# Kernel optimization log

Hardware: AMD Instinct MI355X
Metric: run time of the kernel (lower is better)

Reference implementation:

```python
import jax, jax.numpy as jnp
import numpy as np

D_MODEL = 1024
N_HEADS = 16
D_HEAD = D_MODEL // N_HEADS
WINDOW = 256
SCALE = D_HEAD ** -0.5


def setup_inputs() -> dict:
    key = jax.random.key(0)
    ks = jax.random.split(key, 5)
    B, S = 2, 2048
    x = jax.random.normal(ks[0], (B, S, D_MODEL), dtype=jnp.float32)
    # weights stored as [d_in, d_out] so forward is x @ W + b
    W_qkv = jax.random.normal(ks[1], (D_MODEL, 3 * D_MODEL), dtype=jnp.float32) * (D_MODEL ** -0.5)
    b_qkv = jnp.zeros((3 * D_MODEL,), dtype=jnp.float32)
    W_out = jax.random.normal(ks[2], (D_MODEL, D_MODEL), dtype=jnp.float32) * (D_MODEL ** -0.5)
    b_out = jnp.zeros((D_MODEL,), dtype=jnp.float32)
    return {"x": x, "W_qkv": W_qkv, "b_qkv": b_qkv, "W_out": W_out, "b_out": b_out}


def _window_mask(S):
    # Faithful to source: keep positions where (i <= j) & (i >= j - WINDOW + 1),
    # i = query index (rows), j = key index (cols). (Anti-causal window, as in repo.)
    idx = jnp.arange(S)
    keep = (idx[:, None] <= idx[None, :]) & (idx[:, None] >= idx[None, :] - WINDOW + 1)
    return keep  # [S, S] bool


def reference(x, W_qkv, b_qkv, W_out, b_out):
    B, S, D = x.shape
    qkv = x @ W_qkv + b_qkv                      # [B,S,3D]
    q, k, v = jnp.split(qkv, 3, axis=-1)
    def heads(t):
        return t.reshape(B, S, N_HEADS, D_HEAD).transpose(0, 2, 1, 3)  # [B,H,S,dh]
    q, k, v = heads(q), heads(k), heads(v)
    attn = jnp.einsum('bhid,bhjd->bhij', q, k) * SCALE  # [B,H,S,S]
    keep = _window_mask(S)
    attn = jnp.where(keep[None, None], attn, -jnp.inf)
    attn = jax.nn.softmax(attn, axis=-1)
    # dropout is identity in eval mode
    out = jnp.einsum('bhij,bhjd->bhid', attn, v)        # [B,H,S,dh]
    out = out.transpose(0, 2, 1, 3).reshape(B, S, D)
    return out @ W_out + b_out
```

## Files before the change

### kernel.cpp

```cpp
#include <hip/hip_runtime.h>

typedef __bf16 bf16x8 __attribute__((ext_vector_type(8)));
typedef float f32x4 __attribute__((ext_vector_type(4)));
typedef unsigned short u16x8 __attribute__((ext_vector_type(8)));
typedef unsigned short u16x4 __attribute__((ext_vector_type(4)));

#define MFMA16(a, b, c) __builtin_amdgcn_mfma_f32_16x16x32_bf16((a), (b), (c), 0, 0, 0)

#define WAIT_VM2  asm volatile("s_waitcnt vmcnt(2)" ::: "memory")
#define WAIT_VM0  asm volatile("s_waitcnt vmcnt(0)" ::: "memory")
#define WAIT_LGKM asm volatile("s_waitcnt lgkmcnt(0)" ::: "memory")
#define BAR       __builtin_amdgcn_s_barrier()

__device__ __forceinline__ unsigned short f2bf(float f) {
  union { float f; unsigned int i; } v; v.f = f;
  unsigned int u = v.i;
  u += 0x7fffu + ((u >> 16) & 1u);
  return (unsigned short)(u >> 16);
}

__device__ __forceinline__ void gload16(const void* g, void* l) {
  __builtin_amdgcn_global_load_lds(
      (const __attribute__((address_space(1))) unsigned int*)g,
      (__attribute__((address_space(3))) unsigned int*)l, 16, 0, 0);
}

__global__ __launch_bounds__(256) void convert_x(const float* __restrict__ X,
                                                 unsigned short* __restrict__ Xb) {
  size_t i = (size_t)(blockIdx.x * 256 + threadIdx.x) * 8;
  f32x4 f0 = *(const f32x4*)(X + i);
  f32x4 f1 = *(const f32x4*)(X + i + 4);
  u16x8 t;
#pragma unroll
  for (int j = 0; j < 4; ++j) { t[j] = f2bf(f0[j]); t[4 + j] = f2bf(f1[j]); }
  *(u16x8*)(Xb + i) = t;
}

__global__ __launch_bounds__(256) void transpose_w(const float* __restrict__ W,
                                                   unsigned short* __restrict__ Wt,
                                                   int N) {
  __shared__ unsigned short t[32][33];
  int tx = threadIdx.x & 31, ty = threadIdx.x >> 5;
  int bx = blockIdx.x;
  int by = blockIdx.y;
#pragma unroll
  for (int j = 0; j < 4; ++j) {
    int r = ty + j * 8;
    t[tx][r] = f2bf(W[(size_t)(by * 32 + r) * N + bx * 32 + tx]);
  }
  __syncthreads();
#pragma unroll
  for (int j = 0; j < 4; ++j) {
    int r = ty + j * 8;
    Wt[(size_t)(bx * 32 + r) * 1024 + by * 32 + tx] = t[r][tx];
  }
}

__global__ __launch_bounds__(512) void gemm_bt(
    const unsigned short* __restrict__ A, const unsigned short* __restrict__ Bt,
    const float* __restrict__ bias,
    unsigned short* __restrict__ O0, unsigned short* __restrict__ O1,
    unsigned short* __restrict__ O2, float* __restrict__ OF, int mode) {
  __shared__ __align__(16) unsigned short As0[128 * 32];
  __shared__ __align__(16) unsigned short Bs0[128 * 32];
  __shared__ __align__(16) unsigned short As1[128 * 32];
  __shared__ __align__(16) unsigned short Bs1[128 * 32];

  const int K = 1024;
  int tid = threadIdx.x;
  int lane = tid & 63, wave = tid >> 6, quad = lane >> 4, l16 = lane & 15;
  int wr = wave >> 2, wc = wave & 3;
  int m0 = blockIdx.x * 128, n0 = blockIdx.y * 128;

  int srow = tid >> 2, su = tid & 3;
  const unsigned short* ag = A + (size_t)(m0 + srow) * K + su * 8;
  const unsigned short* bg = Bt + (size_t)(n0 + srow) * K + su * 8;
  int loff = tid * 16;

  int abase = (wr * 64 + l16) * 64 + quad * 16;
  int bbase = (wc * 32 + l16) * 64 + quad * 16;

  f32x4 acc[4][2];
#pragma unroll
  for (int i = 0; i < 4; ++i)
#pragma unroll
    for (int j = 0; j < 2; ++j) acc[i][j] = f32x4{0.f, 0.f, 0.f, 0.f};

  auto STAGE = [&](int k0, char* Asb, char* Bsb) {
    gload16(ag + k0, Asb + loff);
    gload16(bg + k0, Bsb + loff);
  };
  auto COMPUTE = [&](const char* Asb, const char* Bsb) {
    bf16x8 af[4], bfr[2];
#pragma unroll
    for (int t = 0; t < 4; ++t)
      af[t] = *(const bf16x8*)(Asb + abase + t * 1024);
#pragma unroll
    for (int t = 0; t < 2; ++t)
      bfr[t] = *(const bf16x8*)(Bsb + bbase + t * 1024);
#pragma unroll
    for (int mt = 0; mt < 4; ++mt)
#pragma unroll
      for (int nt = 0; nt < 2; ++nt)
        acc[mt][nt] = MFMA16(af[mt], bfr[nt], acc[mt][nt]);
  };

  STAGE(0, (char*)As0, (char*)Bs0);
  for (int t = 0; t < 30; t += 2) {
    STAGE((t + 1) * 32, (char*)As1, (char*)Bs1);
    WAIT_VM2; BAR;
    COMPUTE((const char*)As0, (const char*)Bs0);
    WAIT_LGKM; BAR;
    STAGE((t + 2) * 32, (char*)As0, (char*)Bs0);
    WAIT_VM2; BAR;
    COMPUTE((const char*)As1, (const char*)Bs1);
    WAIT_LGKM; BAR;
  }
  STAGE(31 * 32, (char*)As1, (char*)Bs1);
  WAIT_VM2; BAR;
  COMPUTE((const char*)As0, (const char*)Bs0);
  WAIT_LGKM; BAR;
  WAIT_VM0; BAR;
  COMPUTE((const char*)As1, (const char*)Bs1);

  if (mode == 0) {
#pragma unroll
    for (int nt = 0; nt < 2; ++nt) {
      int n = n0 + wc * 32 + nt * 16 + l16;
      float bv = bias[n];
      int seg = n >> 10, cc = n & 1023, hh = cc >> 6, d = cc & 63;
#pragma unroll
      for (int mt = 0; mt < 4; ++mt) {
        int mb = m0 + wr * 64 + mt * 16 + quad * 4;
        int b = mb >> 11, s = mb & 2047;
        if (seg == 2) {
          u16x4 pk;
#pragma unroll
          for (int r = 0; r < 4; ++r) pk[r] = f2bf(acc[mt][nt][r] + bv);
          *(u16x4*)&O2[((size_t)((b << 4) + hh) * 64 + d) * 2048 + s] = pk;
        } else {
          unsigned short* O = seg ? O1 : O0;
#pragma unroll
          for (int r = 0; r < 4; ++r)
            O[((size_t)((b << 4) + hh) * 2048 + (s + r)) * 64 + d] = f2bf(acc[mt][nt][r] + bv);
        }
      }
    }
  } else {
#pragma unroll
    for (int nt = 0; nt < 2; ++nt) {
      int n = n0 + wc * 32 + nt * 16 + l16;
      float bv = bias[n];
#pragma unroll
      for (int mt = 0; mt < 4; ++mt) {
        int mb = m0 + wr * 64 + mt * 16 + quad * 4;
#pragma unroll
        for (int r = 0; r < 4; ++r)
          OF[(size_t)(mb + r) * 1024 + n] = acc[mt][nt][r] + bv;
      }
    }
  }
}

__global__ __launch_bounds__(256) void gemm_bt64(
    const unsigned short* __restrict__ A, const unsigned short* __restrict__ Bt,
    const float* __restrict__ bias, float* __restrict__ OF) {
  __shared__ __align__(16) unsigned short As0[64 * 32];
  __shared__ __align__(16) unsigned short Bs0[64 * 32];
  __shared__ __align__(16) unsigned short As1[64 * 32];
  __shared__ __align__(16) unsigned short Bs1[64 * 32];

  const int K = 1024;
  int tid = threadIdx.x;
  int lane = tid & 63, wave = tid >> 6, quad = lane >> 4, l16 = lane & 15;
  int wr = wave >> 1, wc = wave & 1;
  int m0 = blockIdx.x * 64, n0 = blockIdx.y * 64;

  int srow = tid >> 2, su = tid & 3;
  const unsigned short* ag = A + (size_t)(m0 + srow) * K + su * 8;
  const unsigned short* bg = Bt + (size_t)(n0 + srow) * K + su * 8;
  int loff = tid * 16;

  int abase = (wr * 32 + l16) * 64 + quad * 16;
  int bbase = (wc * 32 + l16) * 64 + quad * 16;

  f32x4 acc[2][2];
#pragma unroll
  for (int i = 0; i < 2; ++i)
#pragma unroll
    for (int j = 0; j < 2; ++j) acc[i][j] = f32x4{0.f, 0.f, 0.f, 0.f};

  auto STAGE = [&](int k0, char* Asb, char* Bsb) {
    gload16(ag + k0, Asb + loff);
    gload16(bg + k0, Bsb + loff);
  };
  auto COMPUTE = [&](const char* Asb, const char* Bsb) {
    bf16x8 af[2], bfr[2];
#pragma unroll
    for (int t = 0; t < 2; ++t) {
      af[t]  = *(const bf16x8*)(Asb + abase + t * 1024);
      bfr[t] = *(const bf16x8*)(Bsb + bbase + t * 1024);
    }
#pragma unroll
    for (int mt = 0; mt < 2; ++mt)
#pragma unroll
      for (int nt = 0; nt < 2; ++nt)
        acc[mt][nt] = MFMA16(af[mt], bfr[nt], acc[mt][nt]);
  };

  STAGE(0, (char*)As0, (char*)Bs0);
  for (int t = 0; t < 30; t += 2) {
    STAGE((t + 1) * 32, (char*)As1, (char*)Bs1);
    WAIT_VM2; BAR;
    COMPUTE((const char*)As0, (const char*)Bs0);
    WAIT_LGKM; BAR;
    STAGE((t + 2) * 32, (char*)As0, (char*)Bs0);
    WAIT_VM2; BAR;
    COMPUTE((const char*)As1, (const char*)Bs1);
    WAIT_LGKM; BAR;
  }
  STAGE(31 * 32, (char*)As1, (char*)Bs1);
  WAIT_VM2; BAR;
  COMPUTE((const char*)As0, (const char*)Bs0);
  WAIT_LGKM; BAR;
  WAIT_VM0; BAR;
  COMPUTE((const char*)As1, (const char*)Bs1);

#pragma unroll
  for (int nt = 0; nt < 2; ++nt) {
    int n = n0 + wc * 32 + nt * 16 + l16;
    float bv = bias[n];
#pragma unroll
    for (int mt = 0; mt < 2; ++mt) {
      int mb = m0 + wr * 32 + mt * 16 + quad * 4;
#pragma unroll
      for (int r = 0; r < 4; ++r)
        OF[(size_t)(mb + r) * 1024 + n] = acc[mt][nt][r] + bv;
    }
  }
}

__global__ __launch_bounds__(256) void attn_kernel(
    const unsigned short* __restrict__ Q, const unsigned short* __restrict__ Kq,
    const unsigned short* __restrict__ Vt, unsigned short* __restrict__ AO) {
  __shared__ __align__(16) unsigned short Ps[4][16][40];

  int bid = blockIdx.x;
  int qblk = bid & 31, h = (bid >> 5) & 15, b = bid >> 9;
  int q0 = qblk * 64;
  int tid = threadIdx.x, lane = tid & 63, wave = tid >> 6, quad = lane >> 4, l16 = lane & 15;

  const unsigned short* Qb = Q + (size_t)(((b << 4) + h) * 2048) * 64;
  const unsigned short* Kb = Kq + (size_t)(((b << 4) + h) * 2048) * 64;
  const unsigned short* Vb = Vt + (size_t)(((b << 4) + h) * 64) * 2048;

  int qrow = q0 + wave * 16 + l16;
  bf16x8 qf0 = __builtin_bit_cast(bf16x8, *(const u16x8*)&Qb[(size_t)qrow * 64 + quad * 8]);
  bf16x8 qf1 = __builtin_bit_cast(bf16x8, *(const u16x8*)&Qb[(size_t)qrow * 64 + 32 + quad * 8]);

  float mrow[4], lrow[4];
  f32x4 zero = {0.f, 0.f, 0.f, 0.f};
  f32x4 o[4];
#pragma unroll
  for (int i = 0; i < 4; ++i) o[i] = zero;
#pragma unroll
  for (int r = 0; r < 4; ++r) { mrow[r] = -1e30f; lrow[r] = 0.f; }

  const float SCALE = 0.125f;
  int pstart = (wave >= 2) ? 1 : 0;
  int pend = pstart + 8;

  for (int p = pstart; p <= pend; ++p) {
    int kbase = q0 + p * 32;

    f32x4 sc[2];
    __builtin_amdgcn_s_setprio(1);
#pragma unroll
    for (int t = 0; t < 2; ++t) {
      int krow = kbase + t * 16 + l16;
      krow = krow > 2047 ? 2047 : krow;
      bf16x8 kf0 = __builtin_bit_cast(bf16x8, *(const u16x8*)&Kb[(size_t)krow * 64 + quad * 8]);
      bf16x8 kf1 = __builtin_bit_cast(bf16x8, *(const u16x8*)&Kb[(size_t)krow * 64 + 32 + quad * 8]);
      f32x4 z = zero;
      z = MFMA16(qf0, kf0, z);
      z = MFMA16(qf1, kf1, z);
      sc[t] = z;
    }
    __builtin_amdgcn_s_setprio(0);

    float sv[2][4];
#pragma unroll
    for (int t = 0; t < 2; ++t)
#pragma unroll
      for (int r = 0; r < 4; ++r) {
        int kg = kbase + t * 16 + l16;
        int qg = q0 + wave * 16 + quad * 4 + r;
        bool valid = (kg >= qg) && (kg <= qg + 255) && (kg < 2048);
        sv[t][r] = valid ? sc[t][r] * SCALE : -1e30f;
      }
#pragma unroll
    for (int r = 0; r < 4; ++r) {
      float v = fmaxf(sv[0][r], sv[1][r]);
      v = fmaxf(v, __shfl_xor(v, 1));
      v = fmaxf(v, __shfl_xor(v, 2));
      v = fmaxf(v, __shfl_xor(v, 4));
      v = fmaxf(v, __shfl_xor(v, 8));
      float mnew = fmaxf(mrow[r], v);
      float alpha = __expf(mrow[r] - mnew);
      mrow[r] = mnew;
      float p0 = __expf(sv[0][r] - mnew);
      float p1 = __expf(sv[1][r] - mnew);
      p0 = (sv[0][r] > -5e29f) ? p0 : 0.f;
      p1 = (sv[1][r] > -5e29f) ? p1 : 0.f;
      float rs = p0 + p1;
      rs += __shfl_xor(rs, 1);
      rs += __shfl_xor(rs, 2);
      rs += __shfl_xor(rs, 4);
      rs += __shfl_xor(rs, 8);
      lrow[r] = lrow[r] * alpha + rs;
#pragma unroll
      for (int nt = 0; nt < 4; ++nt) o[nt][r] *= alpha;
      Ps[wave][quad * 4 + r][l16] = f2bf(p0);
      Ps[wave][quad * 4 + r][16 + l16] = f2bf(p1);
    }
    __threadfence_block();
    bf16x8 pf = __builtin_bit_cast(bf16x8, *(const u16x8*)&Ps[wave][l16][quad * 8]);

    int vcol = kbase + quad * 8;
    vcol = vcol > 2040 ? 2040 : vcol;
    __builtin_amdgcn_s_setprio(1);
#pragma unroll
    for (int nt = 0; nt < 4; ++nt) {
      int vrow = nt * 16 + l16;
      bf16x8 vf = __builtin_bit_cast(bf16x8, *(const u16x8*)&Vb[(size_t)vrow * 2048 + vcol]);
      o[nt] = MFMA16(pf, vf, o[nt]);
    }
    __builtin_amdgcn_s_setprio(0);
  }

  unsigned short* dst = AO + ((size_t)(b * 2048 + q0 + wave * 16) * 1024) + h * 64;
#pragma unroll
  for (int nt = 0; nt < 4; ++nt)
#pragma unroll
    for (int r = 0; r < 4; ++r) {
      int qq = quad * 4 + r;
      dst[(size_t)qq * 1024 + nt * 16 + l16] = f2bf(o[nt][r] / lrow[r]);
    }
}

extern "C" void kernel_launch(void* const* d_in, const int* in_sizes, int n_in,
                              void* d_out, int out_size, void* d_ws, size_t ws_size,
                              hipStream_t stream) {
  const float* x = (const float*)d_in[0];
  const float* W_qkv = (const float*)d_in[1];
  const float* b_qkv = (const float*)d_in[2];
  const float* W_out = (const float*)d_in[3];
  const float* b_out = (const float*)d_in[4];
  float* out = (float*)d_out;

  unsigned short* ws = (unsigned short*)d_ws;
  unsigned short* Qw  = ws;
  unsigned short* Kw  = ws + 4194304;
  unsigned short* Vw  = ws + 8388608;
  unsigned short* Wqt = ws + 12582912;
  unsigned short* AO  = ws + 12582912;
  unsigned short* Wot = ws;
  unsigned short* Xb  = (unsigned short*)d_out;

  dim3 blk(256);
  dim3 gblk(512);
  convert_x<<<dim3(2048), blk, 0, stream>>>(x, Xb);
  transpose_w<<<dim3(96, 32), blk, 0, stream>>>(W_qkv, Wqt, 3072);
  gemm_bt<<<dim3(32, 24), gblk, 0, stream>>>(Xb, Wqt, b_qkv, Qw, Kw, Vw, nullptr, 0);
  attn_kernel<<<dim3(1024), blk, 0, stream>>>(Qw, Kw, Vw, AO);
  transpose_w<<<dim3(32, 32), blk, 0, stream>>>(W_out, Wot, 1024);
  gemm_bt64<<<dim3(64, 16), blk, 0, stream>>>(AO, Wot, b_out, out);
}
```

Measured before the change: 175.7 us.

## Transpose score MFMA so each lane owns one query row; prefetch V earlier

The QK^T MFMA operands are swapped so the score tile comes out transposed, with each lane holding one query row's scores across keys. The online softmax max and sum then need only two cross-lane shuffles instead of four per row, and per-row alpha is broadcast with shuffles. V fragments are loaded before the softmax to hide their global-load latency. The transposed probabilities are written to LDS as packed 4-element vectors, and the final row sums are exchanged through LDS for normalization. This costs extra shuffles for alpha and an LDS round trip at the end.

```diff
diff --git a/kernel.cpp b/kernel.cpp
--- a/kernel.cpp
+++ b/kernel.cpp
@@ -254,17 +254,15 @@
   const unsigned short* Kb = Kq + (size_t)(((b << 4) + h) * 2048) * 64;
   const unsigned short* Vb = Vt + (size_t)(((b << 4) + h) * 64) * 2048;
 
-  int qrow = q0 + wave * 16 + l16;
-  bf16x8 qf0 = __builtin_bit_cast(bf16x8, *(const u16x8*)&Qb[(size_t)qrow * 64 + quad * 8]);
-  bf16x8 qf1 = __builtin_bit_cast(bf16x8, *(const u16x8*)&Qb[(size_t)qrow * 64 + 32 + quad * 8]);
-
-  float mrow[4], lrow[4];
+  int qg = q0 + wave * 16 + l16;
+  bf16x8 qf0 = __builtin_bit_cast(bf16x8, *(const u16x8*)&Qb[(size_t)qg * 64 + quad * 8]);
+  bf16x8 qf1 = __builtin_bit_cast(bf16x8, *(const u16x8*)&Qb[(size_t)qg * 64 + 32 + quad * 8]);
+
+  float m = -1e30f, l = 0.f;
   f32x4 zero = {0.f, 0.f, 0.f, 0.f};
   f32x4 o[4];
 #pragma unroll
   for (int i = 0; i < 4; ++i) o[i] = zero;
-#pragma unroll
-  for (int r = 0; r < 4; ++r) { mrow[r] = -1e30f; lrow[r] = 0.f; }
 
   const float SCALE = 0.125f;
   int pstart = (wave >= 2) ? 1 : 0;
@@ -282,61 +280,83 @@
       bf16x8 kf0 = __builtin_bit_cast(bf16x8, *(const u16x8*)&Kb[(size_t)krow * 64 + quad * 8]);
       bf16x8 kf1 = __builtin_bit_cast(bf16x8, *(const u16x8*)&Kb[(size_t)krow * 64 + 32 + quad * 8]);
       f32x4 z = zero;
-      z = MFMA16(qf0, kf0, z);
-      z = MFMA16(qf1, kf1, z);
+      z = MFMA16(kf0, qf0, z);
+      z = MFMA16(kf1, qf1, z);
       sc[t] = z;
     }
     __builtin_amdgcn_s_setprio(0);
 
+    bf16x8 vf[4];
+    {
+      int vcol = kbase + quad * 8;
+      vcol = vcol > 2040 ? 2040 : vcol;
+#pragma unroll
+      for (int nt = 0; nt < 4; ++nt)
+        vf[nt] = __builtin_bit_cast(bf16x8,
+            *(const u16x8*)&Vb[(size_t)(nt * 16 + l16) * 2048 + vcol]);
+    }
+
     float sv[2][4];
 #pragma unroll
     for (int t = 0; t < 2; ++t)
 #pragma unroll
       for (int r = 0; r < 4; ++r) {
-        int kg = kbase + t * 16 + l16;
-        int qg = q0 + wave * 16 + quad * 4 + r;
+        int kg = kbase + t * 16 + quad * 4 + r;
         bool valid = (kg >= qg) && (kg <= qg + 255) && (kg < 2048);
         sv[t][r] = valid ? sc[t][r] * SCALE : -1e30f;
       }
-#pragma unroll
-    for (int r = 0; r < 4; ++r) {
-      float v = fmaxf(sv[0][r], sv[1][r]);
-      v = fmaxf(v, __shfl_xor(v, 1));
-      v = fmaxf(v, __shfl_xor(v, 2));
-      v = fmaxf(v, __shfl_xor(v, 4));
-      v = fmaxf(v, __shfl_xor(v, 8));
-      float mnew = fmaxf(mrow[r], v);
-      float alpha = __expf(mrow[r] - mnew);
-      mrow[r] = mnew;
-      float p0 = __expf(sv[0][r] - mnew);
-      float p1 = __expf(sv[1][r] - mnew);
-      p0 = (sv[0][r] > -5e29f) ? p0 : 0.f;
-      p1 = (sv[1][r] > -5e29f) ? p1 : 0.f;
-      float rs = p0 + p1;
-      rs += __shfl_xor(rs, 1);
-      rs += __shfl_xor(rs, 2);
-      rs += __shfl_xor(rs, 4);
-      rs += __shfl_xor(rs, 8);
-      lrow[r] = lrow[r] * alpha + rs;
-#pragma unroll
-      for (int nt = 0; nt < 4; ++nt) o[nt][r] *= alpha;
-      Ps[wave][quad * 4 + r][l16] = f2bf(p0);
-      Ps[wave][quad * 4 + r][16 + l16] = f2bf(p1);
+
+    float vmax = fmaxf(fmaxf(fmaxf(sv[0][0], sv[0][1]), fmaxf(sv[0][2], sv[0][3])),
+                       fmaxf(fmaxf(sv[1][0], sv[1][1]), fmaxf(sv[1][2], sv[1][3])));
+    vmax = fmaxf(vmax, __shfl_xor(vmax, 16));
+    vmax = fmaxf(vmax, __shfl_xor(vmax, 32));
+    float mnew = fmaxf(m, vmax);
+    float alpha = __expf(m - mnew);
+    m = mnew;
+    float pe[2][4];
+#pragma unroll
+    for (int t = 0; t < 2; ++t)
+#pragma unroll
+      for (int r = 0; r < 4; ++r) {
+        float e = __expf(sv[t][r] - mnew);
+        pe[t][r] = (sv[t][r] > -5e29f) ? e : 0.f;
+      }
+    float rs = ((pe[0][0] + pe[0][1]) + (pe[0][2] + pe[0][3])) +
+               ((pe[1][0] + pe[1][1]) + (pe[1][2] + pe[1][3]));
+    rs += __shfl_xor(rs, 16);
+    rs += __shfl_xor(rs, 32);
+    l = l * alpha + rs;
+
+    f32x4 av;
+#pragma unroll
+    for (int r = 0; r < 4; ++r) av[r] = __shfl(alpha, quad * 4 + r);
+#pragma unroll
+    for (int nt = 0; nt < 4; ++nt) o[nt] *= av;
+
+#pragma unroll
+    for (int t = 0; t < 2; ++t) {
+      u16x4 pk;
+#pragma unroll
+      for (int r = 0; r < 4; ++r) pk[r] = f2bf(pe[t][r]);
+      *(u16x4*)&Ps[wave][l16][t * 16 + quad * 4] = pk;
     }
     __threadfence_block();
     bf16x8 pf = __builtin_bit_cast(bf16x8, *(const u16x8*)&Ps[wave][l16][quad * 8]);
 
-    int vcol = kbase + quad * 8;
-    vcol = vcol > 2040 ? 2040 : vcol;
     __builtin_amdgcn_s_setprio(1);
 #pragma unroll
-    for (int nt = 0; nt < 4; ++nt) {
-      int vrow = nt * 16 + l16;
-      bf16x8 vf = __builtin_bit_cast(bf16x8, *(const u16x8*)&Vb[(size_t)vrow * 2048 + vcol]);
-      o[nt] = MFMA16(pf, vf, o[nt]);
-    }
+    for (int nt = 0; nt < 4; ++nt)
+      o[nt] = MFMA16(pf, vf[nt], o[nt]);
     __builtin_amdgcn_s_setprio(0);
   }
+
+  __threadfence_block();
+  float* Lf = (float*)&Ps[wave][0][0];
+  Lf[l16] = l;
+  __threadfence_block();
+  float lr[4];
+#pragma unroll
+  for (int r = 0; r < 4; ++r) lr[r] = Lf[quad * 4 + r];
 
   unsigned short* dst = AO + ((size_t)(b * 2048 + q0 + wave * 16) * 1024) + h * 64;
 #pragma unroll
@@ -344,7 +364,7 @@
 #pragma unroll
     for (int r = 0; r < 4; ++r) {
       int qq = quad * 4 + r;
-      dst[(size_t)qq * 1024 + nt * 16 + l16] = f2bf(o[nt][r] / lrow[r]);
+      dst[(size_t)qq * 1024 + nt * 16 + l16] = f2bf(o[nt][r] / lr[r]);
     }
 }
 
```

Result: no change. 175.7 us (+0.1%).
